# Kernel tuning notes

Measured on AMD Instinct MI355X. Metric: run time of the kernel, lower is better.

The kernel has to match this reference:

```python
import jax, jax.numpy as jnp
import numpy as np

N = 50000
E = 800000
SLOPE = 0.2
# layer dims: (in, heads, out_per_head)
DIMS = [(256, 4, 64), (256, 4, 64), (256, 1, 128)]


def _glorot(key, shape):
    fan_in, fan_out = shape[0], shape[-1]
    lim = (6.0 / (fan_in + fan_out)) ** 0.5
    return jax.random.uniform(key, shape, jnp.float32, -lim, lim)


def setup_inputs() -> dict:
    key = jax.random.key(0)
    ks = jax.random.split(key, 20)
    inp = {
        "x": jax.random.normal(ks[0], (N, 256), jnp.float32),
        "edge_index": jax.random.randint(ks[1], (2, E), 0, N, jnp.int32),
        "edge_attr": jax.random.normal(ks[2], (E, 16), jnp.float32),
    }
    ki = 3
    for l, (din, H, C) in enumerate(DIMS):
        inp[f"W{l}"] = _glorot(ks[ki], (din, H * C)); ki += 1
        inp[f"att_src{l}"] = _glorot(ks[ki], (H, C)); ki += 1
        inp[f"att_dst{l}"] = _glorot(ks[ki], (H, C)); ki += 1
        inp[f"b{l}"] = jnp.zeros((H * C,), jnp.float32)
    return inp


def gat_layer(x, src, dst, W, att_src, att_dst, b, H, C):
    n = x.shape[0]
    h = (x @ W).reshape(n, H, C)                      # [N,H,C]
    a_s = (h * att_src).sum(-1)                       # [N,H]
    a_d = (h * att_dst).sum(-1)                       # [N,H]
    e = jax.nn.leaky_relu(a_s[src] + a_d[dst], SLOPE)  # [E,H]
    m = jax.ops.segment_max(e, dst, num_segments=n)   # segment softmax over dst
    e = jnp.exp(e - jnp.where(jnp.isfinite(m), m, 0.0)[dst])
    denom = jax.ops.segment_sum(e, dst, num_segments=n)
    alpha = e / (denom[dst] + 1e-16)                  # [E,H]
    out = jax.ops.segment_sum(alpha[:, :, None] * h[src], dst, num_segments=n)
    return out.reshape(n, H * C) + b


def reference(x, edge_index, edge_attr, W0, att_src0, att_dst0, b0,
              W1, att_src1, att_dst1, b1, W2, att_src2, att_dst2, b2):
    # edge_attr is unused: GATConv was built without edge_dim (no edge projection).
    src, dst = edge_index[0], edge_index[1]
    h = gat_layer(x, src, dst, W0, att_src0, att_dst0, b0, *DIMS[0][1:])
    h = gat_layer(h, src, dst, W1, att_src1, att_dst1, b1, *DIMS[1][1:])
    h = gat_layer(h, src, dst, W2, att_src2, att_dst2, b2, *DIMS[2][1:])
    return h
```

## Files before the change

### kernel.cpp

```cpp
#include <hip/hip_runtime.h>
#include <math.h>


#define SLOPE 0.2f

__device__ __forceinline__ int wave_incl_scan(int v) {
#pragma unroll
  for (int off = 1; off < 64; off <<= 1) {
    int t = __shfl_up(v, off, 64);
    if ((int)(threadIdx.x & 63) >= off) v += t;
  }
  return v;
}


__global__ void k_hist(const int* __restrict__ dst, int E, int* __restrict__ rowptr) {
  int e = blockIdx.x * blockDim.x + threadIdx.x;
  if (e < E) atomicAdd(&rowptr[dst[e] + 1], 1);
}

__global__ __launch_bounds__(1024) void k_scan_block(int* __restrict__ data, int n,
                                                     int* __restrict__ sums) {
  int tid = threadIdx.x;
  int gid = blockIdx.x * 1024 + tid;
  int v = (gid < n) ? data[gid] : 0;
  int sv = wave_incl_scan(v);
  __shared__ int wsum[16];
  int w = tid >> 6, l = tid & 63;
  if (l == 63) wsum[w] = sv;
  __syncthreads();
  if (w == 0) {
    int x = (l < 16) ? wsum[l] : 0;
    x = wave_incl_scan(x);
    if (l < 16) wsum[l] = x;
  }
  __syncthreads();
  if (w > 0) sv += wsum[w - 1];
  if (gid < n) data[gid] = sv;
  if (tid == 1023 && sums) sums[blockIdx.x] = sv;
}

__global__ void k_scan_add(int* __restrict__ data, int n, const int* __restrict__ sums) {
  int gid = blockIdx.x * blockDim.x + threadIdx.x;
  if (gid < n) {
    int b = gid >> 10;
    if (b > 0) data[gid] += sums[b - 1];
  }
}

__global__ void k_copy_i32(const int* __restrict__ a, int* __restrict__ b, int n) {
  int i = blockIdx.x * blockDim.x + threadIdx.x;
  if (i < n) b[i] = a[i];
}

__global__ void k_scatter(const int* __restrict__ src, const int* __restrict__ dst, int E,
                          int* __restrict__ rowcur, int* __restrict__ permsrc) {
  int e = blockIdx.x * blockDim.x + threadIdx.x;
  if (e < E) {
    int d = dst[e];
    int pos = atomicAdd(&rowcur[d], 1);
    permsrc[pos] = src[e];
  }
}


__global__ __launch_bounds__(256) void k_gemm64(const float* __restrict__ A,
                                                const float* __restrict__ B,
                                                float* __restrict__ C,
                                                int M, int K, int NC) {
  __shared__ float As[16][68];
  __shared__ float Bs[16][64];
  int tid = threadIdx.x;
  int tx = tid & 15, ty = tid >> 4;
  int bm = blockIdx.x * 64, bn = blockIdx.y * 64;
  int ar = tid >> 2;
  int ak = (tid & 3) << 2;
  int bk = tid >> 4;
  int bn4 = (tid & 15) << 2;
  const bool arow_ok = (bm + ar) < M;
  float acc[4][4] = {};
  for (int k0 = 0; k0 < K; k0 += 16) {
    float4 av = make_float4(0.f, 0.f, 0.f, 0.f);
    if (arow_ok) av = *(const float4*)(A + (size_t)(bm + ar) * K + k0 + ak);
    float4 bv = *(const float4*)(B + (size_t)(k0 + bk) * NC + bn + bn4);
    As[ak + 0][ar] = av.x;
    As[ak + 1][ar] = av.y;
    As[ak + 2][ar] = av.z;
    As[ak + 3][ar] = av.w;
    *(float4*)&Bs[bk][bn4] = bv;
    __syncthreads();
#pragma unroll
    for (int k = 0; k < 16; ++k) {
      float4 a = *(const float4*)&As[k][ty << 2];
      float4 b = *(const float4*)&Bs[k][tx << 2];
      acc[0][0] += a.x * b.x; acc[0][1] += a.x * b.y; acc[0][2] += a.x * b.z; acc[0][3] += a.x * b.w;
      acc[1][0] += a.y * b.x; acc[1][1] += a.y * b.y; acc[1][2] += a.y * b.z; acc[1][3] += a.y * b.w;
      acc[2][0] += a.z * b.x; acc[2][1] += a.z * b.y; acc[2][2] += a.z * b.z; acc[2][3] += a.z * b.w;
      acc[3][0] += a.w * b.x; acc[3][1] += a.w * b.y; acc[3][2] += a.w * b.z; acc[3][3] += a.w * b.w;
    }
    __syncthreads();
  }
#pragma unroll
  for (int i = 0; i < 4; ++i) {
    int row = bm + (ty << 2) + i;
    if (row < M) {
      float4 o = make_float4(acc[i][0], acc[i][1], acc[i][2], acc[i][3]);
      *(float4*)(C + (size_t)row * NC + bn + (tx << 2)) = o;
    }
  }
}


template <int H, int C>
__global__ void k_scores(const float* __restrict__ h, const float* __restrict__ att_s,
                         const float* __restrict__ att_d, float* __restrict__ a_s,
                         float* __restrict__ a_d, int Nn) {
  int t = blockIdx.x * blockDim.x + threadIdx.x;
  if (t >= Nn * H) return;
  int n = t / H, hh = t % H;
  const float4* hp = (const float4*)(h + (size_t)n * (H * C) + hh * C);
  const float4* sp = (const float4*)(att_s + hh * C);
  const float4* dp = (const float4*)(att_d + hh * C);
  float s = 0.f, d = 0.f;
#pragma unroll
  for (int c = 0; c < C / 4; ++c) {
    float4 v = hp[c], a = sp[c], b = dp[c];
    s += v.x * a.x + v.y * a.y + v.z * a.z + v.w * a.w;
    d += v.x * b.x + v.y * b.y + v.z * b.z + v.w * b.w;
  }
  a_s[t] = s;
  a_d[t] = d;
}


template <int H>
__global__ void k_softmax(const int* __restrict__ rowptr, const int* __restrict__ permsrc,
                          const float* __restrict__ a_s, const float* __restrict__ a_d,
                          float* __restrict__ m_out, float* __restrict__ inv_den, int Nn) {
  int n = blockIdx.x * blockDim.x + threadIdx.x;
  if (n >= Nn) return;
  int start = rowptr[n], end = rowptr[n + 1];
  float ad[H], m[H], den[H];
  if constexpr (H == 4) {
    float4 v = ((const float4*)a_d)[n];
    ad[0] = v.x; ad[1] = v.y; ad[2] = v.z; ad[3] = v.w;
  } else {
    ad[0] = a_d[n];
  }
#pragma unroll
  for (int h = 0; h < H; ++h) {
    m[h] = -INFINITY;
    den[h] = 0.f;
  }
  for (int p = start; p < end; ++p) {
    int s = permsrc[p];
    float as[H];
    if constexpr (H == 4) {
      float4 v = ((const float4*)a_s)[s];
      as[0] = v.x; as[1] = v.y; as[2] = v.z; as[3] = v.w;
    } else {
      as[0] = a_s[s];
    }
#pragma unroll
    for (int h = 0; h < H; ++h) {
      float e = as[h] + ad[h];
      e = e > 0.f ? e : SLOPE * e;
      float mn = fmaxf(m[h], e);
      den[h] = den[h] * expf(m[h] - mn) + expf(e - mn);
      m[h] = mn;
    }
  }
#pragma unroll
  for (int h = 0; h < H; ++h) {
    m_out[(size_t)n * H + h] = isfinite(m[h]) ? m[h] : 0.f;
    inv_den[(size_t)n * H + h] = 1.f / (den[h] + 1e-16f);
  }
}


template <int H, int C>
__global__ void k_aggregate(const int* __restrict__ rowptr, const int* __restrict__ permsrc,
                            const float* __restrict__ a_s, const float* __restrict__ a_d,
                            const float* __restrict__ m_arr, const float* __restrict__ inv_den,
                            const float* __restrict__ h, const float* __restrict__ bias,
                            float* __restrict__ out, int Nn) {
  constexpr int HC = H * C;
  constexpr int PL = HC / 64;
  int gw = (blockIdx.x * blockDim.x + threadIdx.x) >> 6;
  if (gw >= Nn) return;
  int lane = threadIdx.x & 63;
  int col0 = lane * PL;
  int hh = col0 / C;
  int start = rowptr[gw], end = rowptr[gw + 1];
  float adv = a_d[(size_t)gw * H + hh];
  float mv = m_arr[(size_t)gw * H + hh];
  float idn = inv_den[(size_t)gw * H + hh];
  float acc[PL] = {};
  for (int c0 = start; c0 < end; c0 += 64) {
    int myp = c0 + lane;
    int sv = (myp < end) ? permsrc[myp] : 0;
    int cnt = min(64, end - c0);
    for (int j = 0; j < cnt; ++j) {
      int s = __shfl(sv, j, 64);
      float e = a_s[(size_t)s * H + hh] + adv;
      e = e > 0.f ? e : SLOPE * e;
      float alpha = expf(e - mv) * idn;
      const float* hp = h + (size_t)s * HC + col0;
      if constexpr (PL == 4) {
        float4 v = *(const float4*)hp;
        acc[0] += alpha * v.x;
        acc[1] += alpha * v.y;
        acc[2] += alpha * v.z;
        acc[3] += alpha * v.w;
      } else {
        float2 v = *(const float2*)hp;
        acc[0] += alpha * v.x;
        acc[1] += alpha * v.y;
      }
    }
  }
#pragma unroll
  for (int j = 0; j < PL; ++j)
    out[(size_t)gw * HC + col0 + j] = acc[j] + bias[col0 + j];
}


extern "C" void kernel_launch(void* const* d_in, const int* in_sizes, int n_in,
                              void* d_out, int out_size, void* d_ws, size_t ws_size,
                              hipStream_t stream) {
  const float* x = (const float*)d_in[0];
  const int* ei = (const int*)d_in[1];
  const int Nn = in_sizes[0] / 256;
  const int E = in_sizes[1] / 2;
  const int* srcI = ei;
  const int* dstI = ei + E;

  const float* W[3]   = {(const float*)d_in[3], (const float*)d_in[7],  (const float*)d_in[11]};
  const float* ats[3] = {(const float*)d_in[4], (const float*)d_in[8],  (const float*)d_in[12]};
  const float* atd[3] = {(const float*)d_in[5], (const float*)d_in[9],  (const float*)d_in[13]};
  const float* bia[3] = {(const float*)d_in[6], (const float*)d_in[10], (const float*)d_in[14]};

  char* p = (char*)d_ws;
  auto alloc = [&](size_t bytes) {
    void* r = (void*)p;
    p += (bytes + 255) & ~(size_t)255;
    return r;
  };
  int* rowptr = (int*)alloc((size_t)(Nn + 1) * sizeof(int));
  int* rowcur = (int*)alloc((size_t)Nn * sizeof(int));
  int* permsrc = (int*)alloc((size_t)E * sizeof(int));
  int* ssum = (int*)alloc(1024 * sizeof(int));
  float* hbuf = (float*)alloc((size_t)Nn * 256 * sizeof(float));
  float* buf0 = (float*)alloc((size_t)Nn * 256 * sizeof(float));
  float* a_s = (float*)alloc((size_t)Nn * 4 * sizeof(float));
  float* a_d = (float*)alloc((size_t)Nn * 4 * sizeof(float));
  float* m_arr = (float*)alloc((size_t)Nn * 4 * sizeof(float));
  float* idn = (float*)alloc((size_t)Nn * 4 * sizeof(float));

  hipMemsetAsync(rowptr, 0, (size_t)(Nn + 1) * sizeof(int), stream);
  const int TB = 256;
  k_hist<<<(E + TB - 1) / TB, TB, 0, stream>>>(dstI, E, rowptr);
  int n1 = Nn + 1;
  int nblk = (n1 + 1023) / 1024;
  k_scan_block<<<nblk, 1024, 0, stream>>>(rowptr, n1, ssum);
  k_scan_block<<<1, 1024, 0, stream>>>(ssum, nblk, (int*)nullptr);
  k_scan_add<<<(n1 + TB - 1) / TB, TB, 0, stream>>>(rowptr, n1, ssum);
  k_copy_i32<<<(Nn + TB - 1) / TB, TB, 0, stream>>>(rowptr, rowcur, Nn);
  k_scatter<<<(E + TB - 1) / TB, TB, 0, stream>>>(srcI, dstI, E, rowcur, permsrc);

  const float* xin = x;
  float* outs[3] = {buf0, buf0, (float*)d_out};
  for (int l = 0; l < 3; ++l) {
    const int H = (l == 2) ? 1 : 4;
    const int HC = (l == 2) ? 128 : 256;
    dim3 g((Nn + 63) / 64, HC / 64);
    k_gemm64<<<g, 256, 0, stream>>>(xin, W[l], hbuf, Nn, 256, HC);
    if (H == 4) {
      k_scores<4, 64><<<(Nn * 4 + TB - 1) / TB, TB, 0, stream>>>(hbuf, ats[l], atd[l], a_s, a_d, Nn);
      k_softmax<4><<<(Nn + TB - 1) / TB, TB, 0, stream>>>(rowptr, permsrc, a_s, a_d, m_arr, idn, Nn);
      k_aggregate<4, 64><<<(Nn + 3) / 4, 256, 0, stream>>>(rowptr, permsrc, a_s, a_d, m_arr, idn,
                                                           hbuf, bia[l], outs[l], Nn);
    } else {
      k_scores<1, 128><<<(Nn + TB - 1) / TB, TB, 0, stream>>>(hbuf, ats[l], atd[l], a_s, a_d, Nn);
      k_softmax<1><<<(Nn + TB - 1) / TB, TB, 0, stream>>>(rowptr, permsrc, a_s, a_d, m_arr, idn, Nn);
      k_aggregate<1, 128><<<(Nn + 3) / 4, 256, 0, stream>>>(rowptr, permsrc, a_s, a_d, m_arr, idn,
                                                            hbuf, bia[l], outs[l], Nn);
    }
    xin = outs[l];
  }
}
```

Baseline: 912.8 us.

## Use 128x128 register-tiled GEMM, prefetch gathers, fast exp, fuse rowcur copy

The FP32 GEMM moves from 64x64 tiles with 4x4 per-thread outputs to 128x128 tiles with 8x8 per-thread outputs and a skewed shared-memory layout for B, raising arithmetic intensity and cutting shared-memory traffic per FMA. The aggregation loop software-prefetches the next neighbour's score and feature vector so the gathers overlap with the accumulate. Softmax and aggregation switch to the fast __expf intrinsic, and the rowcur copy is folded into the scan-add kernel to remove one launch. The bigger tile uses more registers and launches fewer blocks, which may lower occupancy, and __expf is slightly less accurate than expf.

After: 873.5 us. -4.3%, faster.

```diff
diff --git a/kernel.cpp b/kernel.cpp
--- a/kernel.cpp
+++ b/kernel.cpp
@@ -40,17 +40,16 @@
   if (tid == 1023 && sums) sums[blockIdx.x] = sv;
 }
 
-__global__ void k_scan_add(int* __restrict__ data, int n, const int* __restrict__ sums) {
+__global__ void k_scan_add(int* __restrict__ data, int n, const int* __restrict__ sums,
+                           int* __restrict__ rowcur, int nrow) {
   int gid = blockIdx.x * blockDim.x + threadIdx.x;
   if (gid < n) {
     int b = gid >> 10;
-    if (b > 0) data[gid] += sums[b - 1];
-  }
-}
-
-__global__ void k_copy_i32(const int* __restrict__ a, int* __restrict__ b, int n) {
-  int i = blockIdx.x * blockDim.x + threadIdx.x;
-  if (i < n) b[i] = a[i];
+    int v = data[gid];
+    if (b > 0) v += sums[b - 1];
+    data[gid] = v;
+    if (gid < nrow) rowcur[gid] = v;
+  }
 }
 
 __global__ void k_scatter(const int* __restrict__ src, const int* __restrict__ dst, int E,
@@ -64,48 +63,65 @@
 }
 
 
-__global__ __launch_bounds__(256) void k_gemm64(const float* __restrict__ A,
-                                                const float* __restrict__ B,
-                                                float* __restrict__ C,
-                                                int M, int K, int NC) {
-  __shared__ float As[16][68];
-  __shared__ float Bs[16][64];
+__device__ __forceinline__ int bskew(int c) { return c + ((c >> 5) << 2); }
+
+__global__ __launch_bounds__(256) void k_gemm128(const float* __restrict__ A,
+                                                 const float* __restrict__ B,
+                                                 float* __restrict__ C,
+                                                 int M, int K, int NC) {
+  __shared__ float As[16][132];
+  __shared__ float Bs[16][140];
   int tid = threadIdx.x;
-  int tx = tid & 15, ty = tid >> 4;
-  int bm = blockIdx.x * 64, bn = blockIdx.y * 64;
-  int ar = tid >> 2;
-  int ak = (tid & 3) << 2;
-  int bk = tid >> 4;
-  int bn4 = (tid & 15) << 2;
-  const bool arow_ok = (bm + ar) < M;
-  float acc[4][4] = {};
+  int bm = blockIdx.x * 128, bn = blockIdx.y * 128;
+  int ar = tid >> 1;
+  int ac = (tid & 1) << 3;
+  int br = tid >> 4;
+  int bc = (tid & 15) << 3;
+  int pbc = bskew(bc);
+  int rowg = (tid >> 4) << 3;
+  int colg = (tid & 15) << 3;
+  int pcolg = bskew(colg);
+  const bool aok = (bm + ar) < M;
+  float acc[8][8] = {};
   for (int k0 = 0; k0 < K; k0 += 16) {
-    float4 av = make_float4(0.f, 0.f, 0.f, 0.f);
-    if (arow_ok) av = *(const float4*)(A + (size_t)(bm + ar) * K + k0 + ak);
-    float4 bv = *(const float4*)(B + (size_t)(k0 + bk) * NC + bn + bn4);
-    As[ak + 0][ar] = av.x;
-    As[ak + 1][ar] = av.y;
-    As[ak + 2][ar] = av.z;
-    As[ak + 3][ar] = av.w;
-    *(float4*)&Bs[bk][bn4] = bv;
+    float4 a0 = make_float4(0.f, 0.f, 0.f, 0.f), a1 = a0;
+    if (aok) {
+      const float* ap = A + (size_t)(bm + ar) * K + k0 + ac;
+      a0 = *(const float4*)ap;
+      a1 = *(const float4*)(ap + 4);
+    }
+    const float* bp = B + (size_t)(k0 + br) * NC + bn + bc;
+    float4 b0 = *(const float4*)bp;
+    float4 b1 = *(const float4*)(bp + 4);
     __syncthreads();
+    As[ac + 0][ar] = a0.x; As[ac + 1][ar] = a0.y;
+    As[ac + 2][ar] = a0.z; As[ac + 3][ar] = a0.w;
+    As[ac + 4][ar] = a1.x; As[ac + 5][ar] = a1.y;
+    As[ac + 6][ar] = a1.z; As[ac + 7][ar] = a1.w;
+    *(float4*)&Bs[br][pbc] = b0;
+    *(float4*)&Bs[br][pbc + 4] = b1;
+    __syncthreads();
 #pragma unroll
     for (int k = 0; k < 16; ++k) {
-      float4 a = *(const float4*)&As[k][ty << 2];
-      float4 b = *(const float4*)&Bs[k][tx << 2];
-      acc[0][0] += a.x * b.x; acc[0][1] += a.x * b.y; acc[0][2] += a.x * b.z; acc[0][3] += a.x * b.w;
-      acc[1][0] += a.y * b.x; acc[1][1] += a.y * b.y; acc[1][2] += a.y * b.z; acc[1][3] += a.y * b.w;
-      acc[2][0] += a.z * b.x; acc[2][1] += a.z * b.y; acc[2][2] += a.z * b.z; acc[2][3] += a.z * b.w;
-      acc[3][0] += a.w * b.x; acc[3][1] += a.w * b.y; acc[3][2] += a.w * b.z; acc[3][3] += a.w * b.w;
-    }
-    __syncthreads();
-  }
-#pragma unroll
-  for (int i = 0; i < 4; ++i) {
-    int row = bm + (ty << 2) + i;
+      float4 a0v = *(const float4*)&As[k][rowg];
+      float4 a1v = *(const float4*)&As[k][rowg + 4];
+      float4 b0v = *(const float4*)&Bs[k][pcolg];
+      float4 b1v = *(const float4*)&Bs[k][pcolg + 4];
+      float av[8] = {a0v.x, a0v.y, a0v.z, a0v.w, a1v.x, a1v.y, a1v.z, a1v.w};
+      float bv[8] = {b0v.x, b0v.y, b0v.z, b0v.w, b1v.x, b1v.y, b1v.z, b1v.w};
+#pragma unroll
+      for (int i = 0; i < 8; ++i)
+#pragma unroll
+        for (int j = 0; j < 8; ++j) acc[i][j] += av[i] * bv[j];
+    }
+  }
+#pragma unroll
+  for (int i = 0; i < 8; ++i) {
+    int row = bm + rowg + i;
     if (row < M) {
-      float4 o = make_float4(acc[i][0], acc[i][1], acc[i][2], acc[i][3]);
-      *(float4*)(C + (size_t)row * NC + bn + (tx << 2)) = o;
+      float* cp = C + (size_t)row * NC + bn + colg;
+      *(float4*)cp = make_float4(acc[i][0], acc[i][1], acc[i][2], acc[i][3]);
+      *(float4*)(cp + 4) = make_float4(acc[i][4], acc[i][5], acc[i][6], acc[i][7]);
     }
   }
 }
@@ -166,7 +182,7 @@
       float e = as[h] + ad[h];
       e = e > 0.f ? e : SLOPE * e;
       float mn = fmaxf(m[h], e);
-      den[h] = den[h] * expf(m[h] - mn) + expf(e - mn);
+      den[h] = den[h] * __expf(m[h] - mn) + __expf(e - mn);
       m[h] = mn;
     }
   }
@@ -200,23 +216,37 @@
     int myp = c0 + lane;
     int sv = (myp < end) ? permsrc[myp] : 0;
     int cnt = min(64, end - c0);
+    int s0 = __shfl(sv, 0, 64);
+    float as0 = a_s[(size_t)s0 * H + hh];
+    float4 v40;
+    float2 v20;
+    if constexpr (PL == 4) v40 = *(const float4*)(h + (size_t)s0 * HC + col0);
+    else                   v20 = *(const float2*)(h + (size_t)s0 * HC + col0);
     for (int j = 0; j < cnt; ++j) {
-      int s = __shfl(sv, j, 64);
-      float e = a_s[(size_t)s * H + hh] + adv;
+      float as1 = 0.f;
+      float4 v41;
+      float2 v21;
+      if (j + 1 < cnt) {
+        int s1 = __shfl(sv, j + 1, 64);
+        as1 = a_s[(size_t)s1 * H + hh];
+        if constexpr (PL == 4) v41 = *(const float4*)(h + (size_t)s1 * HC + col0);
+        else                   v21 = *(const float2*)(h + (size_t)s1 * HC + col0);
+      }
+      float e = as0 + adv;
       e = e > 0.f ? e : SLOPE * e;
-      float alpha = expf(e - mv) * idn;
-      const float* hp = h + (size_t)s * HC + col0;
+      float alpha = __expf(e - mv) * idn;
       if constexpr (PL == 4) {
-        float4 v = *(const float4*)hp;
-        acc[0] += alpha * v.x;
-        acc[1] += alpha * v.y;
-        acc[2] += alpha * v.z;
-        acc[3] += alpha * v.w;
+        acc[0] += alpha * v40.x;
+        acc[1] += alpha * v40.y;
+        acc[2] += alpha * v40.z;
+        acc[3] += alpha * v40.w;
+        v40 = v41;
       } else {
-        float2 v = *(const float2*)hp;
-        acc[0] += alpha * v.x;
-        acc[1] += alpha * v.y;
+        acc[0] += alpha * v20.x;
+        acc[1] += alpha * v20.y;
+        v20 = v21;
       }
+      as0 = as1;
     }
   }
 #pragma unroll
@@ -264,8 +294,7 @@
   int nblk = (n1 + 1023) / 1024;
   k_scan_block<<<nblk, 1024, 0, stream>>>(rowptr, n1, ssum);
   k_scan_block<<<1, 1024, 0, stream>>>(ssum, nblk, (int*)nullptr);
-  k_scan_add<<<(n1 + TB - 1) / TB, TB, 0, stream>>>(rowptr, n1, ssum);
-  k_copy_i32<<<(Nn + TB - 1) / TB, TB, 0, stream>>>(rowptr, rowcur, Nn);
+  k_scan_add<<<(n1 + TB - 1) / TB, TB, 0, stream>>>(rowptr, n1, ssum, rowcur, Nn);
   k_scatter<<<(E + TB - 1) / TB, TB, 0, stream>>>(srcI, dstI, E, rowcur, permsrc);
 
   const float* xin = x;
@@ -273,8 +302,8 @@
   for (int l = 0; l < 3; ++l) {
     const int H = (l == 2) ? 1 : 4;
     const int HC = (l == 2) ? 128 : 256;
-    dim3 g((Nn + 63) / 64, HC / 64);
-    k_gemm64<<<g, 256, 0, stream>>>(xin, W[l], hbuf, Nn, 256, HC);
+    dim3 g((Nn + 127) / 128, HC / 128);
+    k_gemm128<<<g, 256, 0, stream>>>(xin, W[l], hbuf, Nn, 256, HC);
     if (H == 4) {
       k_scores<4, 64><<<(Nn * 4 + TB - 1) / TB, TB, 0, stream>>>(hbuf, ats[l], atd[l], a_s, a_d, Nn);
       k_softmax<4><<<(Nn + TB - 1) / TB, TB, 0, stream>>>(rowptr, permsrc, a_s, a_d, m_arr, idn, Nn);
```
